# Kernel tuning notes

Measured on AMD Instinct MI355X. Metric: run time of the kernel, lower is better.

The kernel has to match this reference:

```python
import jax, jax.numpy as jnp
import numpy as np

NUM_HEADS = 8
ALPHA = 0.01  # leaky_relu slope
MAX_SEQ = 64


def layer_norm(x, g, b, eps=1e-5):
    m = jnp.mean(x, axis=-1, keepdims=True)
    v = jnp.var(x, axis=-1, keepdims=True)
    return (x - m) * jax.lax.rsqrt(v + eps) * g + b


def ff(x, w1, b1, w2, b2):
    # Linear -> exact GELU -> Linear (torch nn.GELU default is erf-based)
    return jax.nn.gelu(x @ w1.T + b1, approximate=False) @ w2.T + b2


def mha(q, k, v, in_w, in_b, out_w, out_b, kpm):
    # torch nn.MultiheadAttention, batch_first=False. q:[Tq,E,d], k/v:[Tk,E,d], kpm:[E,Tk] True=pad
    d = q.shape[-1]
    H = NUM_HEADS
    dh = d // H
    qp = q @ in_w[:d].T + in_b[:d]
    kp = k @ in_w[d:2 * d].T + in_b[d:2 * d]
    vp = v @ in_w[2 * d:].T + in_b[2 * d:]
    Tq, E, _ = qp.shape
    Tk = kp.shape[0]
    qh = qp.reshape(Tq, E, H, dh) * (dh ** -0.5)
    kh = kp.reshape(Tk, E, H, dh)
    vh = vp.reshape(Tk, E, H, dh)
    scores = jnp.einsum('qehd,kehd->ehqk', qh, kh)  # [E,H,Tq,Tk]
    scores = jnp.where(kpm[:, None, None, :], jnp.float32(-1e9), scores)
    att = jax.nn.softmax(scores, axis=-1)
    out = jnp.einsum('ehqk,kehd->qehd', att, vh).reshape(Tq, E, d)
    return out @ out_w.T + out_b


def setup_inputs() -> dict:
    key = jax.random.key(0)
    ks = jax.random.split(key, 40)
    N, d, E, Seq, H = 50000, 64, 150000, 5, NUM_HEADS

    def xn(k, shape, scale):
        return jax.random.normal(k, shape, dtype=jnp.float32) * scale

    inp = {
        'features': xn(ks[0], (N, d), 1.0),
        'pos_emb': xn(ks[1], (MAX_SEQ, d), 0.02),
        'self_in_w': xn(ks[2], (3 * d, d), 0.1),
        'self_in_b': jnp.zeros((3 * d,), jnp.float32),
        'self_out_w': xn(ks[3], (d, d), 0.1),
        'self_out_b': jnp.zeros((d,), jnp.float32),
        'cross_in_w': xn(ks[4], (3 * d, d), 0.1),
        'cross_in_b': jnp.zeros((3 * d,), jnp.float32),
        'cross_out_w': xn(ks[5], (d, d), 0.1),
        'cross_out_b': jnp.zeros((d,), jnp.float32),
        'sa_ln1_g': jnp.ones((d,), jnp.float32), 'sa_ln1_b': jnp.zeros((d,), jnp.float32),
        'sa_ln2_g': jnp.ones((d,), jnp.float32), 'sa_ln2_b': jnp.zeros((d,), jnp.float32),
        'ca_ln1_g': jnp.ones((d,), jnp.float32), 'ca_ln1_b': jnp.zeros((d,), jnp.float32),
        'ca_ln2_g': jnp.ones((d,), jnp.float32), 'ca_ln2_b': jnp.zeros((d,), jnp.float32),
        'sa_ff_w1': xn(ks[6], (4 * d, d), 0.08), 'sa_ff_b1': jnp.zeros((4 * d,), jnp.float32),
        'sa_ff_w2': xn(ks[7], (d, 4 * d), 0.08), 'sa_ff_b2': jnp.zeros((d,), jnp.float32),
        'ca_ff_w1': xn(ks[8], (4 * d, d), 0.08), 'ca_ff_b1': jnp.zeros((4 * d,), jnp.float32),
        'ca_ff_w2': xn(ks[9], (d, 4 * d), 0.08), 'ca_ff_b2': jnp.zeros((d,), jnp.float32),
        'inst_w': xn(ks[10], (NUM_HEADS * d, d), 0.08),
        'attn_vec': xn(ks[11], (1, NUM_HEADS, d), 0.2),
        'edge_metapath_indices': jax.random.randint(ks[12], (E, Seq), 0, N, dtype=jnp.int64)
            if jax.config.jax_enable_x64 else jax.random.randint(ks[12], (E, Seq), 0, N).astype(jnp.int32),
        'dst': jax.random.randint(ks[13], (E,), 0, N).astype(jnp.int32),
    }
    inp['edge_metapath_indices'] = inp['edge_metapath_indices'].astype(jnp.int32)
    return inp


def reference(features, pos_emb, self_in_w, self_in_b, self_out_w, self_out_b,
              cross_in_w, cross_in_b, cross_out_w, cross_out_b,
              sa_ln1_g, sa_ln1_b, sa_ln2_g, sa_ln2_b,
              ca_ln1_g, ca_ln1_b, ca_ln2_g, ca_ln2_b,
              sa_ff_w1, sa_ff_b1, sa_ff_w2, sa_ff_b2,
              ca_ff_w1, ca_ff_b1, ca_ff_w2, ca_ff_b2,
              inst_w, attn_vec, edge_metapath_indices, dst):
    N, d = features.shape
    pad_id = N  # module pads one zero row; indices == pad_id are padding
    feats = jnp.concatenate([features, jnp.zeros((1, d), features.dtype)], axis=0)
    idx = edge_metapath_indices  # [E, Seq]
    E, Seq = idx.shape
    kpm = idx == pad_id  # [E, Seq] key padding mask

    edata = feats[idx]  # [E, Seq, d] gather (embedding)
    tokens = jnp.transpose(edata, (1, 0, 2))  # [Seq, E, d]
    pos_vec = pos_emb[:Seq][:, None, :]  # [Seq, 1, d]
    pos_vec = jnp.where(kpm.T[:, :, None], jnp.float32(0.0), pos_vec)
    tokens = tokens + pos_vec  # pos_drop is identity in eval

    # pre-LN self-attention block over the metapath sequence
    sa_in = layer_norm(tokens, sa_ln1_g, sa_ln1_b)
    tokens = tokens + mha(sa_in, sa_in, sa_in, self_in_w, self_in_b, self_out_w, self_out_b, kpm)
    sa_out = jnp.transpose(tokens, (1, 0, 2))  # [E, Seq, d]

    valid = (~kpm).astype(features.dtype)  # [E, Seq]
    denom = jnp.clip(valid.sum(axis=1, keepdims=True), 1.0, None)
    inst_emb = (sa_out * valid[:, :, None]).sum(axis=1) / denom  # masked mean pool
    inst_emb = inst_emb + ff(layer_norm(inst_emb, sa_ln2_g, sa_ln2_b), sa_ff_w1, sa_ff_b1, sa_ff_w2, sa_ff_b2)

    # cross-attention: last (target) node attends over the sequence
    lengths = (~kpm).sum(axis=1)
    last_pos = jnp.clip(lengths - 1, 0, None)
    last_ids = jnp.take_along_axis(idx, last_pos[:, None], axis=1)[:, 0]
    target_feat = feats[last_ids]
    q = layer_norm(target_feat, ca_ln1_g, ca_ln1_b)[None]  # [1, E, d]
    cross_out = mha(q, tokens, tokens, cross_in_w, cross_in_b, cross_out_w, cross_out_b, kpm)
    inst_emb = inst_emb + cross_out[0]
    inst_emb = inst_emb + ff(layer_norm(inst_emb, ca_ln2_g, ca_ln2_b), ca_ff_w1, ca_ff_b1, ca_ff_w2, ca_ff_b2)

    # heads projection, leaky-relu attention score, edge softmax, scatter-sum
    eft = (inst_emb @ inst_w.T).reshape(E, NUM_HEADS, d)  # [E, H, d]
    a = jnp.sum(eft * attn_vec, axis=-1)  # [E, H]
    a = jnp.where(a > 0, a, ALPHA * a)  # leaky_relu
    seg_max = jax.ops.segment_max(a, dst, num_segments=N)  # per-dst-node max
    a_exp = jnp.exp(a - seg_max[dst])
    seg_sum = jax.ops.segment_sum(a_exp, dst, num_segments=N)
    att = a_exp / seg_sum[dst]  # edge_softmax; attn_drop=0 -> identity
    ret = jax.ops.segment_sum(eft * att[:, :, None], dst, num_segments=N)  # [N, H, d]
    return ret
```

## Files before the change

### kernel.cpp

```cpp
#include <hip/hip_runtime.h>
#include <math.h>

#define D 64
#define LOG2E 1.44269504088896340736f
#define QSCALE (0.35355339059327373f * LOG2E)

typedef float f32x4 __attribute__((ext_vector_type(4)));
typedef float vf4 __attribute__((ext_vector_type(4)));
typedef short bf16x8 __attribute__((ext_vector_type(8)));
typedef unsigned short ushort_t;

#define MF(a, b, c) __builtin_amdgcn_mfma_f32_16x16x32_bf16(a, b, c, 0, 0, 0)

__device__ __forceinline__ float bcast(float x, int i) {
  return __int_as_float(__builtin_amdgcn_readlane(__float_as_int(x), i));
}
__device__ __forceinline__ float qsum(float x) {
  x += __shfl_xor(x, 16);
  x += __shfl_xor(x, 32);
  return x;
}
__device__ __forceinline__ ushort_t f2b(float f) {
  unsigned int u = __float_as_uint(f);
  unsigned int r = (u + 0x7FFFu + ((u >> 16) & 1u)) >> 16;
  return (ushort_t)r;
}
__device__ __forceinline__ float b2f(short s) {
  return __uint_as_float(((unsigned int)(unsigned short)s) << 16);
}
__device__ __forceinline__ f32x4 ld4(const float* __restrict__ p) { return *(const f32x4*)p; }
__device__ __forceinline__ unsigned int fkey(float f) {
  unsigned int b = __float_as_uint(f);
  return (b & 0x80000000u) ? ~b : (b | 0x80000000u);
}
__device__ __forceinline__ float funkey(unsigned int k) {
  return __uint_as_float((k & 0x80000000u) ? (k ^ 0x80000000u) : ~k);
}
__device__ __forceinline__ bf16x8 mkpair(const f32x4& ce, const f32x4& co) {
  bf16x8 b;
#pragma unroll
  for (int j = 0; j < 4; j++) {
    b[j] = (short)f2b(ce[j]);
    b[4 + j] = (short)f2b(co[j]);
  }
  return b;
}
__device__ __forceinline__ f32x4 unpk(bf16x8 p, int half) {
  f32x4 r;
#pragma unroll
  for (int j = 0; j < 4; j++) r[j] = b2f(p[half * 4 + j]);
  return r;
}

__device__ __forceinline__ void lnT(const f32x4 (&x)[4], f32x4 (&y)[4],
                                    const float* __restrict__ g, const float* __restrict__ b,
                                    int quad) {
  float s1 = 0.f, s2 = 0.f;
#pragma unroll
  for (int ct = 0; ct < 4; ct++)
#pragma unroll
    for (int r = 0; r < 4; r++) { s1 += x[ct][r]; s2 += x[ct][r] * x[ct][r]; }
  s1 = qsum(s1);
  s2 = qsum(s2);
  float mean = s1 * 0.015625f;
  float var = s2 * 0.015625f - mean * mean;
  float rs = rsqrtf(var + 1e-5f);
#pragma unroll
  for (int ct = 0; ct < 4; ct++) {
    f32x4 gv = ld4(g + 16 * ct + 4 * quad);
    f32x4 bv = ld4(b + 16 * ct + 4 * quad);
#pragma unroll
    for (int r = 0; r < 4; r++) y[ct][r] = (x[ct][r] - mean) * rs * gv[r] + bv[r];
  }
}

__global__ void zero_kernel(float4* __restrict__ p, int n4) {
  int t = blockIdx.x * blockDim.x + threadIdx.x;
  if (t < n4) p[t] = make_float4(0.f, 0.f, 0.f, 0.f);
}

__global__ void prep_kernel(const float* __restrict__ si, const float* __restrict__ so,
                            const float* __restrict__ w1s, const float* __restrict__ w2s,
                            const float* __restrict__ ci, const float* __restrict__ co,
                            const float* __restrict__ w1c, const float* __restrict__ w2c,
                            const float* __restrict__ iw, const float* __restrict__ av,
                            float* __restrict__ ws) {
  int t = blockIdx.x * blockDim.x + threadIdx.x;
  ushort_t* bw = (ushort_t*)(ws + 33280);
  if (t < 98304) {
    const float* src;
    int base, cs;
    int l = t;
    if      (l < 12288) { src = si;  base = 0;     cs = 6; }
    else if (l < 16384) { src = so;  base = 12288; cs = 6; l -= 12288; }
    else if (l < 32768) { src = w1s; base = 16384; cs = 6; l -= 16384; }
    else if (l < 49152) { src = w2s; base = 32768; cs = 8; l -= 32768; }
    else if (l < 61440) { src = ci;  base = 49152; cs = 6; l -= 49152; }
    else if (l < 65536) { src = co;  base = 61440; cs = 6; l -= 61440; }
    else if (l < 81920) { src = w1c; base = 65536; cs = 6; l -= 65536; }
    else                { src = w2c; base = 81920; cs = 8; l -= 81920; }
    int c = l >> cs, k = l & ((1 << cs) - 1);
    int T = (1 << cs) >> 5;
    int ct = c >> 4, m = c & 15, tt = k >> 5, rem = k & 31;
    int quad = (rem >> 2) & 3;
    int j = (((rem >> 4) & 1) << 2) | (rem & 3);
    bw[base + (size_t)((ct * T + tt) * 64 + quad * 16 + m) * 8 + j] = f2b(src[l]);
  } else if (t < 131072) {
    int l = t - 98304;
    int c = l >> 6, k = l & 63;
    ws[(k >> 2) * 2048 + c * 4 + (k & 3)] = iw[l];
  } else if (t < 131584) {
    int l = t - 131072;
    int h = l >> 6, k = l & 63;
    float acc = 0.f;
    for (int c = 0; c < 64; c++) acc += av[h * 64 + c] * iw[(h * 64 + c) * 64 + k];
    ws[32768 + h * 64 + k] = acc;
  }
}

__device__ __forceinline__ void ffnT(f32x4 (&inst)[4],
                                     const float* __restrict__ g, const float* __restrict__ b,
                                     const bf16x8* __restrict__ W1, const bf16x8* __restrict__ W2,
                                     const float* __restrict__ b1, const float* __restrict__ b2,
                                     int lane, int quad) {
  f32x4 y[4];
  lnT(inst, y, g, b, quad);
  bf16x8 x0 = mkpair(y[0], y[1]), x1 = mkpair(y[2], y[3]);
  bf16x8 Hp[8];
#pragma unroll
  for (int ht = 0; ht < 8; ht++) {
    f32x4 h[2];
#pragma unroll
    for (int u = 0; u < 2; u++) {
      int ct = 2 * ht + u;
      f32x4 c = {0.f, 0.f, 0.f, 0.f};
      c = MF(W1[(ct * 2 + 0) * 64 + lane], x0, c);
      c = MF(W1[(ct * 2 + 1) * 64 + lane], x1, c);
      f32x4 bb = ld4(b1 + 16 * ct + 4 * quad);
#pragma unroll
      for (int r = 0; r < 4; r++) {
        float v = c[r] + bb[r];
        h[u][r] = 0.5f * v * (1.0f + erff(v * 0.70710678118654752440f));
      }
    }
    Hp[ht] = mkpair(h[0], h[1]);
  }
#pragma unroll
  for (int ct = 0; ct < 4; ct++) {
    f32x4 c = {0.f, 0.f, 0.f, 0.f};
#pragma unroll
    for (int t = 0; t < 8; t++) c = MF(W2[(ct * 8 + t) * 64 + lane], Hp[t], c);
    f32x4 bb = ld4(b2 + 16 * ct + 4 * quad);
#pragma unroll
    for (int r = 0; r < 4; r++) inst[ct][r] += c[r] + bb[r];
  }
}

__global__ __launch_bounds__(64, 2)
void edge_kernel(const float* __restrict__ features, const float* __restrict__ pos_emb,
                 const float* __restrict__ self_in_b, const float* __restrict__ self_out_b,
                 const float* __restrict__ cross_in_b, const float* __restrict__ cross_out_b,
                 const float* __restrict__ sa_ln1_g, const float* __restrict__ sa_ln1_b,
                 const float* __restrict__ sa_ln2_g, const float* __restrict__ sa_ln2_b,
                 const float* __restrict__ ca_ln1_g, const float* __restrict__ ca_ln1_b,
                 const float* __restrict__ ca_ln2_g, const float* __restrict__ ca_ln2_b,
                 const float* __restrict__ sa_ff_b1, const float* __restrict__ sa_ff_b2,
                 const float* __restrict__ ca_ff_b1, const float* __restrict__ ca_ff_b2,
                 const int* __restrict__ midx, const int* __restrict__ dstv,
                 const float* __restrict__ ws,
                 float* __restrict__ inst_out, float* __restrict__ a_out,
                 unsigned int* __restrict__ seg_max, int E, int N) {
  const int lane = threadIdx.x;
  const int quad = lane >> 4, lo = lane & 15;
  const int e0 = blockIdx.x * 16;
  __shared__ float xp[16 * 68];

  const ushort_t* bw = (const ushort_t*)(ws + 33280);
  const bf16x8* WSI = (const bf16x8*)(bw);
  const bf16x8* WSO = (const bf16x8*)(bw + 12288);
  const bf16x8* W1S = (const bf16x8*)(bw + 16384);
  const bf16x8* W2S = (const bf16x8*)(bw + 32768);
  const bf16x8* WCI = (const bf16x8*)(bw + 49152);
  const bf16x8* WCO = (const bf16x8*)(bw + 61440);
  const bf16x8* W1C = (const bf16x8*)(bw + 65536);
  const bf16x8* W2C = (const bf16x8*)(bw + 81920);
  const float* uvec = ws + 32768;

  const bool ge = (e0 + lo) < E;
  const int eIdx = min(e0 + lo, E - 1);
  int ids[5];
#pragma unroll
  for (int s = 0; s < 5; s++) ids[s] = midx[eIdx * 5 + s];
  int vb = 0;
#pragma unroll
  for (int s = 0; s < 5; s++)
    if (ids[s] != N && ge) vb |= (1 << s);
  const int nv = __popc(vb);
  const int lp = max(nv - 1, 0);
  int lid = ids[0];
#pragma unroll
  for (int s = 1; s < 5; s++) lid = (lp == s) ? ids[s] : lid;

  bf16x8 XL[5][2];
#pragma unroll
  for (int s = 0; s < 5; s++) {
    f32x4 t[4], y[4];
    const bool vd = (vb >> s) & 1;
    const float* fp = features + (size_t)min(ids[s], N - 1) * 64;
#pragma unroll
    for (int ct = 0; ct < 4; ct++) {
      f32x4 f = ld4(fp + 16 * ct + 4 * quad);
      f32x4 p = ld4(pos_emb + s * 64 + 16 * ct + 4 * quad);
#pragma unroll
      for (int r = 0; r < 4; r++) t[ct][r] = vd ? (f[r] + p[r]) : 0.f;
    }
    lnT(t, y, sa_ln1_g, sa_ln1_b, quad);
    XL[s][0] = mkpair(y[0], y[1]);
    XL[s][1] = mkpair(y[2], y[3]);
  }

  bf16x8 Kp[5][2], Vp[5][2];
#pragma unroll
  for (int s = 0; s < 5; s++) {
    f32x4 kt[4], vt[4];
#pragma unroll
    for (int ct = 0; ct < 4; ct++) {
      f32x4 c = {0.f, 0.f, 0.f, 0.f};
      c = MF(WSI[((4 + ct) * 2 + 0) * 64 + lane], XL[s][0], c);
      c = MF(WSI[((4 + ct) * 2 + 1) * 64 + lane], XL[s][1], c);
      f32x4 bb = ld4(self_in_b + 64 + 16 * ct + 4 * quad);
#pragma unroll
      for (int r = 0; r < 4; r++) kt[ct][r] = c[r] + bb[r];
      f32x4 c2 = {0.f, 0.f, 0.f, 0.f};
      c2 = MF(WSI[((8 + ct) * 2 + 0) * 64 + lane], XL[s][0], c2);
      c2 = MF(WSI[((8 + ct) * 2 + 1) * 64 + lane], XL[s][1], c2);
      f32x4 bb2 = ld4(self_in_b + 128 + 16 * ct + 4 * quad);
#pragma unroll
      for (int r = 0; r < 4; r++) vt[ct][r] = c2[r] + bb2[r];
    }
    Kp[s][0] = mkpair(kt[0], kt[1]);
    Kp[s][1] = mkpair(kt[2], kt[3]);
    Vp[s][0] = mkpair(vt[0], vt[1]);
    Vp[s][1] = mkpair(vt[2], vt[3]);
  }

  f32x4 pool[4];
#pragma unroll
  for (int ct = 0; ct < 4; ct++) pool[ct] = (f32x4){0.f, 0.f, 0.f, 0.f};
  bf16x8 TP[5][2];
#pragma unroll
  for (int qs = 0; qs < 5; qs++) {
    f32x4 qf[4];
#pragma unroll
    for (int ct = 0; ct < 4; ct++) {
      f32x4 c = {0.f, 0.f, 0.f, 0.f};
      c = MF(WSI[(ct * 2 + 0) * 64 + lane], XL[qs][0], c);
      c = MF(WSI[(ct * 2 + 1) * 64 + lane], XL[qs][1], c);
      f32x4 bb = ld4(self_in_b + 16 * ct + 4 * quad);
#pragma unroll
      for (int r = 0; r < 4; r++) qf[ct][r] = (c[r] + bb[r]) * QSCALE;
    }
    float p[4][5];
#pragma unroll
    for (int ct = 0; ct < 4; ct++) {
      float mx = -3.0e30f;
#pragma unroll
      for (int ks = 0; ks < 5; ks++) {
        f32x4 kv = unpk(Kp[ks][ct >> 1], ct & 1);
        float sp = qf[ct][0] * kv[0] + qf[ct][1] * kv[1] + qf[ct][2] * kv[2] + qf[ct][3] * kv[3];
        sp += __shfl_xor(sp, 16);
        float sv = ((vb >> ks) & 1) ? sp : -1e30f;
        p[ct][ks] = sv;
        mx = fmaxf(mx, sv);
      }
      float sum = 0.f;
#pragma unroll
      for (int ks = 0; ks < 5; ks++) { p[ct][ks] = exp2f(p[ct][ks] - mx); sum += p[ct][ks]; }
      float ri = 1.0f / sum;
#pragma unroll
      for (int ks = 0; ks < 5; ks++) p[ct][ks] *= ri;
    }
    f32x4 o[4];
#pragma unroll
    for (int ct = 0; ct < 4; ct++) {
      o[ct] = (f32x4){0.f, 0.f, 0.f, 0.f};
#pragma unroll
      for (int ks = 0; ks < 5; ks++) {
        f32x4 vv = unpk(Vp[ks][ct >> 1], ct & 1);
#pragma unroll
        for (int r = 0; r < 4; r++) o[ct][r] = fmaf(p[ct][ks], vv[r], o[ct][r]);
      }
    }
    bf16x8 o0 = mkpair(o[0], o[1]), o1 = mkpair(o[2], o[3]);
    const bool vd = (vb >> qs) & 1;
    const float* fp = features + (size_t)min(ids[qs], N - 1) * 64;
    f32x4 tpc[4];
#pragma unroll
    for (int ct = 0; ct < 4; ct++) {
      f32x4 c = {0.f, 0.f, 0.f, 0.f};
      c = MF(WSO[(ct * 2 + 0) * 64 + lane], o0, c);
      c = MF(WSO[(ct * 2 + 1) * 64 + lane], o1, c);
      f32x4 bb = ld4(self_out_b + 16 * ct + 4 * quad);
      f32x4 f = ld4(fp + 16 * ct + 4 * quad);
      f32x4 pp = ld4(pos_emb + qs * 64 + 16 * ct + 4 * quad);
#pragma unroll
      for (int r = 0; r < 4; r++) {
        float tokr = vd ? (f[r] + pp[r]) : 0.f;
        float tp = c[r] + bb[r] + tokr;
        tpc[ct][r] = tp;
        pool[ct][r] += vd ? tp : 0.f;
      }
    }
    TP[qs][0] = mkpair(tpc[0], tpc[1]);
    TP[qs][1] = mkpair(tpc[2], tpc[3]);
  }

  f32x4 inst[4];
  {
    float rn = 1.0f / (float)max(nv, 1);
#pragma unroll
    for (int ct = 0; ct < 4; ct++)
#pragma unroll
      for (int r = 0; r < 4; r++) inst[ct][r] = pool[ct][r] * rn;
  }

  ffnT(inst, sa_ln2_g, sa_ln2_b, W1S, W2S, sa_ff_b1, sa_ff_b2, lane, quad);

  {
    f32x4 tf[4], xq[4];
    const bool vdl = lid != N;
    const float* fp = features + (size_t)min(lid, N - 1) * 64;
#pragma unroll
    for (int ct = 0; ct < 4; ct++) {
      f32x4 f = ld4(fp + 16 * ct + 4 * quad);
#pragma unroll
      for (int r = 0; r < 4; r++) tf[ct][r] = vdl ? f[r] : 0.f;
    }
    lnT(tf, xq, ca_ln1_g, ca_ln1_b, quad);
    bf16x8 xq0 = mkpair(xq[0], xq[1]), xq1 = mkpair(xq[2], xq[3]);
    f32x4 qcf[4];
#pragma unroll
    for (int ct = 0; ct < 4; ct++) {
      f32x4 c = {0.f, 0.f, 0.f, 0.f};
      c = MF(WCI[(ct * 2 + 0) * 64 + lane], xq0, c);
      c = MF(WCI[(ct * 2 + 1) * 64 + lane], xq1, c);
      f32x4 bb = ld4(cross_in_b + 16 * ct + 4 * quad);
#pragma unroll
      for (int r = 0; r < 4; r++) qcf[ct][r] = (c[r] + bb[r]) * QSCALE;
    }
    bf16x8 Kc[5][2], Vc[5][2];
#pragma unroll
    for (int s = 0; s < 5; s++) {
      f32x4 kt[4], vt[4];
#pragma unroll
      for (int ct = 0; ct < 4; ct++) {
        f32x4 c = {0.f, 0.f, 0.f, 0.f};
        c = MF(WCI[((4 + ct) * 2 + 0) * 64 + lane], TP[s][0], c);
        c = MF(WCI[((4 + ct) * 2 + 1) * 64 + lane], TP[s][1], c);
        f32x4 bb = ld4(cross_in_b + 64 + 16 * ct + 4 * quad);
#pragma unroll
        for (int r = 0; r < 4; r++) kt[ct][r] = c[r] + bb[r];
        f32x4 c2 = {0.f, 0.f, 0.f, 0.f};
        c2 = MF(WCI[((8 + ct) * 2 + 0) * 64 + lane], TP[s][0], c2);
        c2 = MF(WCI[((8 + ct) * 2 + 1) * 64 + lane], TP[s][1], c2);
        f32x4 bb2 = ld4(cross_in_b + 128 + 16 * ct + 4 * quad);
#pragma unroll
        for (int r = 0; r < 4; r++) vt[ct][r] = c2[r] + bb2[r];
      }
      Kc[s][0] = mkpair(kt[0], kt[1]);
      Kc[s][1] = mkpair(kt[2], kt[3]);
      Vc[s][0] = mkpair(vt[0], vt[1]);
      Vc[s][1] = mkpair(vt[2], vt[3]);
    }
    float p[4][5];
#pragma unroll
    for (int ct = 0; ct < 4; ct++) {
      float mx = -3.0e30f;
#pragma unroll
      for (int ks = 0; ks < 5; ks++) {
        f32x4 kv = unpk(Kc[ks][ct >> 1], ct & 1);
        float sp = qcf[ct][0] * kv[0] + qcf[ct][1] * kv[1] + qcf[ct][2] * kv[2] + qcf[ct][3] * kv[3];
        sp += __shfl_xor(sp, 16);
        float sv = ((vb >> ks) & 1) ? sp : -1e30f;
        p[ct][ks] = sv;
        mx = fmaxf(mx, sv);
      }
      float sum = 0.f;
#pragma unroll
      for (int ks = 0; ks < 5; ks++) { p[ct][ks] = exp2f(p[ct][ks] - mx); sum += p[ct][ks]; }
      float ri = 1.0f / sum;
#pragma unroll
      for (int ks = 0; ks < 5; ks++) p[ct][ks] *= ri;
    }
    f32x4 co[4];
#pragma unroll
    for (int ct = 0; ct < 4; ct++) {
      co[ct] = (f32x4){0.f, 0.f, 0.f, 0.f};
#pragma unroll
      for (int ks = 0; ks < 5; ks++) {
        f32x4 vv = unpk(Vc[ks][ct >> 1], ct & 1);
#pragma unroll
        for (int r = 0; r < 4; r++) co[ct][r] = fmaf(p[ct][ks], vv[r], co[ct][r]);
      }
    }
    bf16x8 c0 = mkpair(co[0], co[1]), c1 = mkpair(co[2], co[3]);
#pragma unroll
    for (int ct = 0; ct < 4; ct++) {
      f32x4 c = {0.f, 0.f, 0.f, 0.f};
      c = MF(WCO[(ct * 2 + 0) * 64 + lane], c0, c);
      c = MF(WCO[(ct * 2 + 1) * 64 + lane], c1, c);
      f32x4 bb = ld4(cross_out_b + 16 * ct + 4 * quad);
#pragma unroll
      for (int r = 0; r < 4; r++) inst[ct][r] += c[r] + bb[r];
    }
  }

  ffnT(inst, ca_ln2_g, ca_ln2_b, W1C, W2C, ca_ff_b1, ca_ff_b2, lane, quad);

  float a8[8];
#pragma unroll
  for (int h = 0; h < 8; h++) {
    float sp = 0.f;
#pragma unroll
    for (int ct = 0; ct < 4; ct++) {
      f32x4 uu = ld4(uvec + h * 64 + 16 * ct + 4 * quad);
#pragma unroll
      for (int r = 0; r < 4; r++) sp = fmaf(inst[ct][r], uu[r], sp);
    }
    sp = qsum(sp);
    a8[h] = sp > 0.f ? sp : 0.01f * sp;
  }
  if (ge) {
    int dd = dstv[e0 + lo];
    float v0 = quad == 0 ? a8[0] : quad == 1 ? a8[2] : quad == 2 ? a8[4] : a8[6];
    float v1 = quad == 0 ? a8[1] : quad == 1 ? a8[3] : quad == 2 ? a8[5] : a8[7];
    atomicMax(&seg_max[dd * 8 + 2 * quad], fkey(v0));
    atomicMax(&seg_max[dd * 8 + 2 * quad + 1], fkey(v1));
    if (quad < 2) {
      f32x4 st = (quad == 0) ? (f32x4){a8[0], a8[1], a8[2], a8[3]}
                             : (f32x4){a8[4], a8[5], a8[6], a8[7]};
      *(f32x4*)(a_out + (size_t)(e0 + lo) * 8 + 4 * quad) = st;
    }
  }

#pragma unroll
  for (int ct = 0; ct < 4; ct++)
    *(f32x4*)(&xp[lo * 68 + 16 * ct + 4 * quad]) = inst[ct];
  __syncthreads();
  {
    int er = lane >> 2, cb = (lane & 3) * 16;
    if (e0 + er < E) {
#pragma unroll
      for (int u = 0; u < 4; u++) {
        f32x4 v = *(const f32x4*)(&xp[er * 68 + cb + 4 * u]);
        *(f32x4*)(inst_out + (size_t)(e0 + er) * 64 + cb + 4 * u) = v;
      }
    }
  }
}

__global__ void expsum_kernel(const float* __restrict__ a, const int* __restrict__ dstv,
                              const unsigned int* __restrict__ seg_max,
                              float* __restrict__ seg_sum, int E8) {
  int t = blockIdx.x * blockDim.x + threadIdx.x;
  if (t >= E8) return;
  int e = t >> 3, h = t & 7;
  int dd = dstv[e];
  float m = funkey(seg_max[dd * 8 + h]);
  atomicAdd(&seg_sum[dd * 8 + h], __expf(a[t] - m));
}

__global__ __launch_bounds__(256)
void scatter_kernel(const float* __restrict__ inst_emb, const float* __restrict__ a,
                    const unsigned int* __restrict__ seg_max, const float* __restrict__ seg_sum,
                    const int* __restrict__ dstv, float* __restrict__ out, int E) {
  const int wid = (blockIdx.x * blockDim.x + threadIdx.x) >> 6;
  const int lane = threadIdx.x & 63;
  if (wid >= E) return;
  int dd = dstv[wid];
  float iv = inst_emb[(size_t)wid * D + lane];
#pragma unroll
  for (int h = 0; h < 8; h++) {
    float m = funkey(seg_max[dd * 8 + h]);
    float s = seg_sum[dd * 8 + h];
    float att = __expf(a[wid * 8 + h] - m) / s;
    atomicAdd(&out[(size_t)dd * 512 + h * 64 + lane], att * iv);
  }
}

__global__ __launch_bounds__(256)
void head_transform_kernel(const float* __restrict__ T_iw, float* __restrict__ out, int N) {
  const int wid = (blockIdx.x * blockDim.x + threadIdx.x) >> 6;
  const int lane = threadIdx.x & 63;
  const int h = wid & 7;
  const int n0 = (wid >> 3) * 4;
  if (n0 >= N) return;
  float z[4], acc[4];
#pragma unroll
  for (int j = 0; j < 4; j++) {
    z[j] = (n0 + j < N) ? out[((size_t)(n0 + j) * 8 + h) * D + lane] : 0.f;
    acc[j] = 0.f;
  }
  const vf4* P = (const vf4*)T_iw;
  for (int k4 = 0; k4 < 16; k4++) {
    vf4 w = P[k4 * 512 + h * 64 + lane];
#pragma unroll
    for (int u = 0; u < 4; u++) {
      int i = k4 * 4 + u;
#pragma unroll
      for (int j = 0; j < 4; j++) acc[j] = fmaf(bcast(z[j], i), w[u], acc[j]);
    }
  }
#pragma unroll
  for (int j = 0; j < 4; j++)
    if (n0 + j < N) out[((size_t)(n0 + j) * 8 + h) * D + lane] = acc[j];
}

extern "C" void kernel_launch(void* const* d_in, const int* in_sizes, int n_in,
                              void* d_out, int out_size, void* d_ws, size_t ws_size,
                              hipStream_t stream) {
  const float* features   = (const float*)d_in[0];
  const float* pos_emb    = (const float*)d_in[1];
  const float* self_in_w  = (const float*)d_in[2];
  const float* self_in_b  = (const float*)d_in[3];
  const float* self_out_w = (const float*)d_in[4];
  const float* self_out_b = (const float*)d_in[5];
  const float* cross_in_w = (const float*)d_in[6];
  const float* cross_in_b = (const float*)d_in[7];
  const float* cross_out_w= (const float*)d_in[8];
  const float* cross_out_b= (const float*)d_in[9];
  const float* sa_ln1_g = (const float*)d_in[10];
  const float* sa_ln1_b = (const float*)d_in[11];
  const float* sa_ln2_g = (const float*)d_in[12];
  const float* sa_ln2_b = (const float*)d_in[13];
  const float* ca_ln1_g = (const float*)d_in[14];
  const float* ca_ln1_b = (const float*)d_in[15];
  const float* ca_ln2_g = (const float*)d_in[16];
  const float* ca_ln2_b = (const float*)d_in[17];
  const float* sa_ff_w1 = (const float*)d_in[18];
  const float* sa_ff_b1 = (const float*)d_in[19];
  const float* sa_ff_w2 = (const float*)d_in[20];
  const float* sa_ff_b2 = (const float*)d_in[21];
  const float* ca_ff_w1 = (const float*)d_in[22];
  const float* ca_ff_b1 = (const float*)d_in[23];
  const float* ca_ff_w2 = (const float*)d_in[24];
  const float* ca_ff_b2 = (const float*)d_in[25];
  const float* inst_w   = (const float*)d_in[26];
  const float* attn_vec = (const float*)d_in[27];
  const int* midx = (const int*)d_in[28];
  const int* dstv = (const int*)d_in[29];

  const int N = in_sizes[0] / 64;
  const int E = in_sizes[29];

  float* wsf = (float*)d_ws;
  float* inst_emb = wsf + 131072;
  float* a_arr = inst_emb + (size_t)E * 64;
  unsigned int* seg_max = (unsigned int*)(a_arr + (size_t)E * 8);
  float* seg_sum = (float*)(seg_max + (size_t)N * 8);

  {
    int n4 = out_size / 4;
    zero_kernel<<<(n4 + 255) / 256, 256, 0, stream>>>((float4*)d_out, n4);
    int s4 = (N * 16) / 4;
    zero_kernel<<<(s4 + 255) / 256, 256, 0, stream>>>((float4*)seg_max, s4);
  }

  prep_kernel<<<(131584 + 255) / 256, 256, 0, stream>>>(
      self_in_w, self_out_w, sa_ff_w1, sa_ff_w2, cross_in_w, cross_out_w, ca_ff_w1, ca_ff_w2,
      inst_w, attn_vec, wsf);

  int nblk = (E + 15) / 16;
  edge_kernel<<<nblk, 64, 0, stream>>>(
      features, pos_emb, self_in_b, self_out_b, cross_in_b, cross_out_b, sa_ln1_g, sa_ln1_b,
      sa_ln2_g, sa_ln2_b, ca_ln1_g, ca_ln1_b, ca_ln2_g, ca_ln2_b, sa_ff_b1, sa_ff_b2, ca_ff_b1,
      ca_ff_b2, midx, dstv, wsf, inst_emb, a_arr, seg_max, E, N);

  expsum_kernel<<<(E * 8 + 255) / 256, 256, 0, stream>>>(a_arr, dstv, seg_max, seg_sum, E * 8);

  scatter_kernel<<<(E + 3) / 4, 256, 0, stream>>>(inst_emb, a_arr, seg_max, seg_sum, dstv,
                                                  (float*)d_out, E);

  int hwave = ((N + 3) / 4) * 8;
  head_transform_kernel<<<(hwave + 3) / 4, 256, 0, stream>>>(wsf, (float*)d_out, N);
}
```

Baseline: 1.028 ms.

## Fold softmax denominator into scatter and head transform; spill TP tokens to LDS

Removes the separate expsum kernel. Scatter now accumulates the unnormalized exp-weighted embeddings and the per-segment exp sums together, and head_transform divides by the segment sum before the projection. In edge_kernel the TP token tiles move from registers to shared memory, and launch bounds drop to one wave minimum per EU so the compiler has more registers to work with. The risks are lower occupancy and extra LDS traffic. There are also slightly different numerics from normalizing after accumulation.

```diff
diff --git a/kernel.cpp b/kernel.cpp
--- a/kernel.cpp
+++ b/kernel.cpp
@@ -156,7 +156,7 @@
   }
 }
 
-__global__ __launch_bounds__(64, 2)
+__global__ __launch_bounds__(64, 1)
 void edge_kernel(const float* __restrict__ features, const float* __restrict__ pos_emb,
                  const float* __restrict__ self_in_b, const float* __restrict__ self_out_b,
                  const float* __restrict__ cross_in_b, const float* __restrict__ cross_out_b,
@@ -174,6 +174,8 @@
   const int quad = lane >> 4, lo = lane & 15;
   const int e0 = blockIdx.x * 16;
   __shared__ float xp[16 * 68];
+  __shared__ __align__(16) ushort_t tpb[10 * 64 * 8];
+  bf16x8* TPB = (bf16x8*)tpb;
 
   const ushort_t* bw = (const ushort_t*)(ws + 33280);
   const bf16x8* WSI = (const bf16x8*)(bw);
@@ -247,7 +249,6 @@
   f32x4 pool[4];
 #pragma unroll
   for (int ct = 0; ct < 4; ct++) pool[ct] = (f32x4){0.f, 0.f, 0.f, 0.f};
-  bf16x8 TP[5][2];
 #pragma unroll
   for (int qs = 0; qs < 5; qs++) {
     f32x4 qf[4];
@@ -311,8 +312,8 @@
         pool[ct][r] += vd ? tp : 0.f;
       }
     }
-    TP[qs][0] = mkpair(tpc[0], tpc[1]);
-    TP[qs][1] = mkpair(tpc[2], tpc[3]);
+    TPB[(qs * 2 + 0) * 64 + lane] = mkpair(tpc[0], tpc[1]);
+    TPB[(qs * 2 + 1) * 64 + lane] = mkpair(tpc[2], tpc[3]);
   }
 
   f32x4 inst[4];
@@ -351,18 +352,20 @@
     bf16x8 Kc[5][2], Vc[5][2];
 #pragma unroll
     for (int s = 0; s < 5; s++) {
+      bf16x8 tp0 = TPB[(s * 2 + 0) * 64 + lane];
+      bf16x8 tp1 = TPB[(s * 2 + 1) * 64 + lane];
       f32x4 kt[4], vt[4];
 #pragma unroll
       for (int ct = 0; ct < 4; ct++) {
         f32x4 c = {0.f, 0.f, 0.f, 0.f};
-        c = MF(WCI[((4 + ct) * 2 + 0) * 64 + lane], TP[s][0], c);
-        c = MF(WCI[((4 + ct) * 2 + 1) * 64 + lane], TP[s][1], c);
+        c = MF(WCI[((4 + ct) * 2 + 0) * 64 + lane], tp0, c);
+        c = MF(WCI[((4 + ct) * 2 + 1) * 64 + lane], tp1, c);
         f32x4 bb = ld4(cross_in_b + 64 + 16 * ct + 4 * quad);
 #pragma unroll
         for (int r = 0; r < 4; r++) kt[ct][r] = c[r] + bb[r];
         f32x4 c2 = {0.f, 0.f, 0.f, 0.f};
-        c2 = MF(WCI[((8 + ct) * 2 + 0) * 64 + lane], TP[s][0], c2);
-        c2 = MF(WCI[((8 + ct) * 2 + 1) * 64 + lane], TP[s][1], c2);
+        c2 = MF(WCI[((8 + ct) * 2 + 0) * 64 + lane], tp0, c2);
+        c2 = MF(WCI[((8 + ct) * 2 + 1) * 64 + lane], tp1, c2);
         f32x4 bb2 = ld4(cross_in_b + 128 + 16 * ct + 4 * quad);
 #pragma unroll
         for (int r = 0; r < 4; r++) vt[ct][r] = c2[r] + bb2[r];
@@ -459,20 +462,9 @@
   }
 }
 
-__global__ void expsum_kernel(const float* __restrict__ a, const int* __restrict__ dstv,
-                              const unsigned int* __restrict__ seg_max,
-                              float* __restrict__ seg_sum, int E8) {
-  int t = blockIdx.x * blockDim.x + threadIdx.x;
-  if (t >= E8) return;
-  int e = t >> 3, h = t & 7;
-  int dd = dstv[e];
-  float m = funkey(seg_max[dd * 8 + h]);
-  atomicAdd(&seg_sum[dd * 8 + h], __expf(a[t] - m));
-}
-
 __global__ __launch_bounds__(256)
 void scatter_kernel(const float* __restrict__ inst_emb, const float* __restrict__ a,
-                    const unsigned int* __restrict__ seg_max, const float* __restrict__ seg_sum,
+                    const unsigned int* __restrict__ seg_max, float* __restrict__ seg_sum,
                     const int* __restrict__ dstv, float* __restrict__ out, int E) {
   const int wid = (blockIdx.x * blockDim.x + threadIdx.x) >> 6;
   const int lane = threadIdx.x & 63;
@@ -482,14 +474,15 @@
 #pragma unroll
   for (int h = 0; h < 8; h++) {
     float m = funkey(seg_max[dd * 8 + h]);
-    float s = seg_sum[dd * 8 + h];
-    float att = __expf(a[wid * 8 + h] - m) / s;
-    atomicAdd(&out[(size_t)dd * 512 + h * 64 + lane], att * iv);
+    float ex = __expf(a[(size_t)wid * 8 + h] - m);
+    if (lane == h) atomicAdd(&seg_sum[dd * 8 + h], ex);
+    atomicAdd(&out[(size_t)dd * 512 + h * 64 + lane], ex * iv);
   }
 }
 
 __global__ __launch_bounds__(256)
-void head_transform_kernel(const float* __restrict__ T_iw, float* __restrict__ out, int N) {
+void head_transform_kernel(const float* __restrict__ T_iw, const float* __restrict__ seg_sum,
+                           float* __restrict__ out, int N) {
   const int wid = (blockIdx.x * blockDim.x + threadIdx.x) >> 6;
   const int lane = threadIdx.x & 63;
   const int h = wid & 7;
@@ -498,7 +491,9 @@
   float z[4], acc[4];
 #pragma unroll
   for (int j = 0; j < 4; j++) {
-    z[j] = (n0 + j < N) ? out[((size_t)(n0 + j) * 8 + h) * D + lane] : 0.f;
+    float s = (n0 + j < N) ? seg_sum[(size_t)(n0 + j) * 8 + h] : 0.f;
+    float rs = s > 0.f ? 1.0f / s : 0.f;
+    z[j] = (n0 + j < N) ? out[((size_t)(n0 + j) * 8 + h) * D + lane] * rs : 0.f;
     acc[j] = 0.f;
   }
   const vf4* P = (const vf4*)T_iw;
@@ -576,11 +571,9 @@
       sa_ln2_g, sa_ln2_b, ca_ln1_g, ca_ln1_b, ca_ln2_g, ca_ln2_b, sa_ff_b1, sa_ff_b2, ca_ff_b1,
       ca_ff_b2, midx, dstv, wsf, inst_emb, a_arr, seg_max, E, N);
 
-  expsum_kernel<<<(E * 8 + 255) / 256, 256, 0, stream>>>(a_arr, dstv, seg_max, seg_sum, E * 8);
-
   scatter_kernel<<<(E + 3) / 4, 256, 0, stream>>>(inst_emb, a_arr, seg_max, seg_sum, dstv,
                                                   (float*)d_out, E);
 
   int hwave = ((N + 3) / 4) * 8;
-  head_transform_kernel<<<(hwave + 3) / 4, 256, 0, stream>>>(wsf, (float*)d_out, N);
-}
+  head_transform_kernel<<<(hwave + 3) / 4, 256, 0, stream>>>(wsf, seg_sum, (float*)d_out, N);
+}
```

New measurement: 1.136 ms. 1.1x slower.
